# Kernel optimization log

Measured on AMD Instinct MI355X. Metric: run time of the kernel, lower is better.

Reference implementation:

```python
import jax, jax.numpy as jnp
import numpy as np

K, A, DIM = 1024, 16384, 512


def setup_inputs() -> dict:
    key = jax.random.key(0)
    ks = jax.random.split(key, 8)
    B, H, W = 2048, 8, 8
    z_t = jax.random.randint(ks[0], (B, H, W), 0, K, dtype=jnp.int64)
    z_tp1 = jax.random.randint(ks[1], (B, H, W), 0, K, dtype=jnp.int64)
    embed_w = jax.random.normal(ks[2], (K, DIM), dtype=jnp.float32) * 0.02
    # MLP: Linear(2*dim -> dim), GELU, Linear(dim -> dim)
    lim1 = 1.0 / np.sqrt(2 * DIM)
    w1 = jax.random.uniform(ks[3], (2 * DIM, DIM), minval=-lim1, maxval=lim1, dtype=jnp.float32)
    b1 = jax.random.uniform(ks[4], (DIM,), minval=-lim1, maxval=lim1, dtype=jnp.float32)
    lim2 = 1.0 / np.sqrt(DIM)
    w2 = jax.random.uniform(ks[5], (DIM, DIM), minval=-lim2, maxval=lim2, dtype=jnp.float32)
    b2 = jax.random.uniform(ks[6], (DIM,), minval=-lim2, maxval=lim2, dtype=jnp.float32)
    codebook_w = jax.random.normal(ks[7], (A, DIM), dtype=jnp.float32) * 0.02
    return {"z_t": z_t, "z_tp1": z_tp1, "embed_w": embed_w, "w1": w1, "b1": b1,
            "w2": w2, "b2": b2, "codebook_w": codebook_w}


def reference(z_t, z_tp1, embed_w, w1, b1, w2, b2, codebook_w):
    B = z_t.shape[0]
    # embed int code grids and mean-pool over H*W tokens -> [B, dim]
    e_t = embed_w[z_t.reshape(B, -1)].mean(axis=1)
    e_tp1 = embed_w[z_tp1.reshape(B, -1)].mean(axis=1)
    h = jnp.concatenate([e_t, e_tp1], axis=-1)          # [B, 2*dim]
    h = jax.nn.gelu(h @ w1 + b1, approximate=False)
    e = h @ w2 + b2                                      # [B, dim]
    # VQ: squared L2 distance to each code, argmin, gather
    d2 = (jnp.sum(e * e, axis=1, keepdims=True)
          - 2.0 * e @ codebook_w.T
          + jnp.sum(codebook_w * codebook_w, axis=1)[None, :])  # [B, A]
    ids = jnp.argmin(d2, axis=1)                         # [B]
    q = codebook_w[ids]                                  # [B, dim]
    return ids, q
```

## Files before the change

### kernel.cpp

```cpp
#include <hip/hip_runtime.h>
#include <hip/hip_bf16.h>

#define TOK 64
#define DIMC 512

typedef __attribute__((ext_vector_type(8))) short v8s;
typedef __attribute__((ext_vector_type(4))) float v4f;

__device__ __forceinline__ unsigned int f2ord(float f) {
  unsigned int u = __float_as_uint(f);
  return (u & 0x80000000u) ? ~u : (u | 0x80000000u);
}

__device__ __forceinline__ float gelu_exact(float x) {
  return 0.5f * x * (1.0f + erff(x * 0.70710678118654752440f));
}

__device__ __forceinline__ unsigned short f2bf(float x) {
  unsigned int u = __float_as_uint(x);
  return (unsigned short)((u + 0x7FFFu + ((u >> 16) & 1u)) >> 16);
}
__device__ __forceinline__ float bf2f(unsigned short h) {
  return __uint_as_float((unsigned int)h << 16);
}

__device__ __forceinline__ void gl2lds16(const void* g, void* l) {
  __builtin_amdgcn_global_load_lds((const __attribute__((address_space(1))) void*)g,
                                   (__attribute__((address_space(3))) void*)l,
                                   16, 0, 0);
}

__global__ __launch_bounds__(256) void k_prep(
    const int* __restrict__ zt, const int* __restrict__ ztp,
    const float* __restrict__ emb,
    unsigned short* __restrict__ hh, unsigned short* __restrict__ hl,
    unsigned long long* __restrict__ rowmin,
    const float* __restrict__ w1, unsigned short* __restrict__ w1th,
    unsigned short* __restrict__ w1tl,
    const float* __restrict__ w2, unsigned short* __restrict__ w2th,
    unsigned short* __restrict__ w2tl,
    const float* __restrict__ cb, unsigned short* __restrict__ ch,
    unsigned short* __restrict__ cl, float* __restrict__ cnorm) {
  __shared__ int codes[128];
  __shared__ float tbuf[32][33];
  const int bid = blockIdx.x;
  const int tid = threadIdx.x;

  if (bid < 2048) {
    const int b = bid;
    if (tid < 64) codes[tid] = zt[b * TOK + tid];
    else if (tid < 128) codes[tid] = ztp[b * TOK + (tid - 64)];
    if (tid == 0) rowmin[b] = 0xFFFFFFFFFFFFFFFFull;
    __syncthreads();
    const int half = tid >> 7;
    const int c4 = tid & 127;
    const float4* emb4 = (const float4*)emb;
    float4 s = make_float4(0.f, 0.f, 0.f, 0.f);
    #pragma unroll 8
    for (int t = 0; t < TOK; t++) {
      const int code = codes[half * TOK + t];
      const float4 v = emb4[code * 128 + c4];
      s.x += v.x; s.y += v.y; s.z += v.z; s.w += v.w;
    }
    const float inv = 1.0f / 64.0f;
    float f[4] = {s.x * inv, s.y * inv, s.z * inv, s.w * inv};
    unsigned short hi[4], lo[4];
    #pragma unroll
    for (int i = 0; i < 4; i++) {
      hi[i] = f2bf(f[i]);
      lo[i] = f2bf(f[i] - bf2f(hi[i]));
    }
    const int off = b * 1024 + half * 512 + c4 * 4;
    *(ushort4*)&hh[off] = make_ushort4(hi[0], hi[1], hi[2], hi[3]);
    *(ushort4*)&hl[off] = make_ushort4(lo[0], lo[1], lo[2], lo[3]);
  } else if (bid < 2816) {
    const float* w; unsigned short *wth, *wtl; int Kd, N, k0, n0;
    if (bid < 2560) {
      const int i = bid - 2048;
      w = w1; wth = w1th; wtl = w1tl; Kd = 1024; N = 512;
      k0 = (i & 31) * 32; n0 = (i >> 5) * 32;
    } else {
      const int i = bid - 2560;
      w = w2; wth = w2th; wtl = w2tl; Kd = 512; N = 512;
      k0 = (i & 15) * 32; n0 = (i >> 4) * 32;
    }
    const int c = tid & 31, r = tid >> 5;
    #pragma unroll
    for (int i = 0; i < 4; i++)
      tbuf[r + i * 8][c] = w[(size_t)(k0 + r + i * 8) * N + n0 + c];
    __syncthreads();
    #pragma unroll
    for (int i = 0; i < 4; i++) {
      const float v = tbuf[c][r + i * 8];
      const unsigned short hi = f2bf(v);
      const unsigned short lo = f2bf(v - bf2f(hi));
      wth[(size_t)(n0 + r + i * 8) * Kd + k0 + c] = hi;
      wtl[(size_t)(n0 + r + i * 8) * Kd + k0 + c] = lo;
    }
  } else {
    const int row = (bid - 2816) * 4 + (tid >> 6);
    const int lane = tid & 63;
    const float4* cb4 = (const float4*)cb;
    const float4 va = cb4[row * 128 + lane * 2];
    const float4 vb = cb4[row * 128 + lane * 2 + 1];
    float s = va.x * va.x + va.y * va.y + va.z * va.z + va.w * va.w
            + vb.x * vb.x + vb.y * vb.y + vb.z * vb.z + vb.w * vb.w;
    float f[8] = {va.x, va.y, va.z, va.w, vb.x, vb.y, vb.z, vb.w};
    unsigned short hi[8], lo[8];
    #pragma unroll
    for (int i = 0; i < 8; i++) {
      hi[i] = f2bf(f[i]);
      lo[i] = f2bf(f[i] - bf2f(hi[i]));
    }
    ushort4* chp = (ushort4*)&ch[row * DIMC + lane * 8];
    ushort4* clp = (ushort4*)&cl[row * DIMC + lane * 8];
    chp[0] = make_ushort4(hi[0], hi[1], hi[2], hi[3]);
    chp[1] = make_ushort4(hi[4], hi[5], hi[6], hi[7]);
    clp[0] = make_ushort4(lo[0], lo[1], lo[2], lo[3]);
    clp[1] = make_ushort4(lo[4], lo[5], lo[6], lo[7]);
    #pragma unroll
    for (int off = 32; off > 0; off >>= 1) s += __shfl_down(s, off);
    if (lane == 0) cnorm[row] = s;
  }
}

template <bool GELU>
__global__ __launch_bounds__(256) void k_gemm(const unsigned short* __restrict__ Ah_,
                                              const unsigned short* __restrict__ Al_,
                                              const unsigned short* __restrict__ Bh_,
                                              const unsigned short* __restrict__ Bl_,
                                              const float* __restrict__ bias,
                                              unsigned short* __restrict__ oh,
                                              unsigned short* __restrict__ ol,
                                              int Kd, int N) {
  __shared__ unsigned short AhS[2][32 * 32];
  __shared__ unsigned short AlS[2][32 * 32];
  __shared__ unsigned short BhS[2][64 * 32];
  __shared__ unsigned short BlS[2][64 * 32];

  const int tid = threadIdx.x;
  const int lane = tid & 63;
  const int wid = tid >> 6;
  const int m0 = blockIdx.x * 32;
  const int n0 = blockIdx.y * 64;

  const unsigned short* Ab_h = Ah_ + (size_t)m0 * Kd;
  const unsigned short* Ab_l = Al_ + (size_t)m0 * Kd;
  const unsigned short* Bb_h = Bh_ + (size_t)n0 * Kd;
  const unsigned short* Bb_l = Bl_ + (size_t)n0 * Kd;

  const int srow = lane >> 2;
  const int sk = (lane & 3) * 8;
  const int wm = wid >> 1, wn = wid & 1;
  const int fr = lane & 15;
  const int fq = (lane >> 4) * 8;

  v4f acc[2];
  acc[0] = (v4f)(0.f);
  acc[1] = (v4f)(0.f);

  auto stage = [&](int b, int k0) {
    #pragma unroll
    for (int u = 0; u < 3; u++) {
      const int i = wid * 3 + u;
      const unsigned short* gs; unsigned short* ls; int rbase;
      if (i < 2)      { gs = Ab_h; ls = AhS[b]; rbase = i * 16; }
      else if (i < 4) { gs = Ab_l; ls = AlS[b]; rbase = (i - 2) * 16; }
      else if (i < 8) { gs = Bb_h; ls = BhS[b]; rbase = (i - 4) * 16; }
      else            { gs = Bb_l; ls = BlS[b]; rbase = (i - 8) * 16; }
      gl2lds16(gs + (size_t)(rbase + srow) * Kd + k0 + sk, ls + rbase * 32);
    }
  };

  stage(0, 0);
  int cur = 0;
  for (int k0 = 0; k0 < Kd; k0 += 32) {
    __syncthreads();
    if (k0 + 32 < Kd) stage(cur ^ 1, k0 + 32);

    const int ar = (wm * 16 + fr) * 32 + fq;
    const v8s ah = *(const v8s*)&AhS[cur][ar];
    const v8s al = *(const v8s*)&AlS[cur][ar];
    #pragma unroll
    for (int nt = 0; nt < 2; nt++) {
      const int br = (wn * 32 + nt * 16 + fr) * 32 + fq;
      const v8s bh = *(const v8s*)&BhS[cur][br];
      const v8s bl = *(const v8s*)&BlS[cur][br];
      acc[nt] = __builtin_amdgcn_mfma_f32_16x16x32_bf16(ah, bh, acc[nt], 0, 0, 0);
      acc[nt] = __builtin_amdgcn_mfma_f32_16x16x32_bf16(ah, bl, acc[nt], 0, 0, 0);
      acc[nt] = __builtin_amdgcn_mfma_f32_16x16x32_bf16(al, bh, acc[nt], 0, 0, 0);
    }
    cur ^= 1;
  }

  const int col16 = lane & 15;
  const int q = lane >> 4;
  #pragma unroll
  for (int nt = 0; nt < 2; nt++) {
    const int col = n0 + wn * 32 + nt * 16 + col16;
    const float bv = bias[col];
    #pragma unroll
    for (int reg = 0; reg < 4; reg++) {
      const int row = m0 + wm * 16 + q * 4 + reg;
      float v = acc[nt][reg] + bv;
      if (GELU) v = gelu_exact(v);
      const unsigned short hi = f2bf(v);
      oh[(size_t)row * N + col] = hi;
      ol[(size_t)row * N + col] = f2bf(v - bf2f(hi));
    }
  }
}

__global__ __launch_bounds__(512, 2) void k_vq(const unsigned short* __restrict__ eh,
                                               const unsigned short* __restrict__ el,
                                               const unsigned short* __restrict__ ch,
                                               const unsigned short* __restrict__ cl,
                                               const float* __restrict__ cnorm,
                                               unsigned long long* __restrict__ rowmin) {
  __shared__ unsigned short lds[2 * 32768];

  const int tid = threadIdx.x;
  const int lane = tid & 63;
  const int wid = tid >> 6;
  const int bid = blockIdx.x;
  const int x = (bid >> 3) & 7;
  const int y = (((bid >> 6) & 7) << 3) | (bid & 7);
  const int r0 = x * 256;
  const int c0 = y * 256;

  const unsigned short* ehB = eh + (size_t)r0 * DIMC;
  const unsigned short* elB = el + (size_t)r0 * DIMC;
  const unsigned short* chB = ch + (size_t)c0 * DIMC;
  const unsigned short* clB = cl + (size_t)c0 * DIMC;

  const int srow = lane >> 2;
  const int sk = (lane & 3) * 8;
  const int wm = wid >> 1;
  const int wn = wid & 1;
  const int fr = lane & 15;
  const int q = lane >> 4;
  const int fq = q * 8;

  v4f acc[4][8];
  #pragma unroll
  for (int i = 0; i < 4; i++)
    #pragma unroll
    for (int jj = 0; jj < 8; jj++) acc[i][jj] = (v4f)(0.f);

  const unsigned short* gp[8];
  int lo_[8];
  #pragma unroll
  for (int u = 0; u < 8; u++) {
    const int i = wid * 8 + u;
    const unsigned short* gs; int off, rbase;
    if (i < 16)      { gs = ehB; off = 0;     rbase = i * 16; }
    else if (i < 32) { gs = elB; off = 8192;  rbase = (i - 16) * 16; }
    else if (i < 48) { gs = chB; off = 16384; rbase = (i - 32) * 16; }
    else             { gs = clB; off = 24576; rbase = (i - 48) * 16; }
    gp[u] = gs + (size_t)(rbase + srow) * DIMC + sk;
    lo_[u] = off + rbase * 32;
  }

  auto stage = [&](int buf, int k0) {
    #pragma unroll
    for (int u = 0; u < 8; u++)
      gl2lds16(gp[u] + k0, lds + buf * 32768 + lo_[u]);
  };

  stage(0, 0);
  __syncthreads();

  for (int t = 0; t < 16; ++t) {
    if (t < 15) stage((t + 1) & 1, (t + 1) * 32);

    const unsigned short* base = lds + (t & 1) * 32768;
    v8s ah[4], al[4];
    #pragma unroll
    for (int mt = 0; mt < 4; mt++) {
      const int ar = (wm * 64 + mt * 16 + fr) * 32 + fq;
      ah[mt] = *(const v8s*)&base[ar];
      al[mt] = *(const v8s*)&base[8192 + ar];
    }
    __builtin_amdgcn_s_setprio(1);
    #pragma unroll
    for (int nt = 0; nt < 8; nt++) {
      const int br = (wn * 128 + nt * 16 + fr) * 32 + fq;
      const v8s bh = *(const v8s*)&base[16384 + br];
      const v8s bl = *(const v8s*)&base[24576 + br];
      #pragma unroll
      for (int mt = 0; mt < 4; mt++) {
        acc[mt][nt] = __builtin_amdgcn_mfma_f32_16x16x32_bf16(ah[mt], bh, acc[mt][nt], 0, 0, 0);
        acc[mt][nt] = __builtin_amdgcn_mfma_f32_16x16x32_bf16(ah[mt], bl, acc[mt][nt], 0, 0, 0);
        acc[mt][nt] = __builtin_amdgcn_mfma_f32_16x16x32_bf16(al[mt], bh, acc[mt][nt], 0, 0, 0);
      }
    }
    __builtin_amdgcn_s_setprio(0);
    if (t < 15) __syncthreads();
  }

  const int col16 = lane & 15;
  float cn[8];
  #pragma unroll
  for (int nt = 0; nt < 8; nt++) cn[nt] = cnorm[c0 + wn * 128 + nt * 16 + col16];

  #pragma unroll
  for (int mt = 0; mt < 4; mt++) {
    #pragma unroll
    for (int reg = 0; reg < 4; reg++) {
      const int row = r0 + wm * 64 + mt * 16 + q * 4 + reg;
      float best = fmaf(-2.f, acc[mt][0][reg], cn[0]);
      int bid2 = c0 + wn * 128 + col16;
      #pragma unroll
      for (int nt = 1; nt < 8; nt++) {
        const float s = fmaf(-2.f, acc[mt][nt][reg], cn[nt]);
        const int id = c0 + wn * 128 + nt * 16 + col16;
        if (s < best) { best = s; bid2 = id; }
      }
      unsigned long long v =
          ((unsigned long long)f2ord(best) << 32) | (unsigned int)bid2;
      #pragma unroll
      for (int off = 8; off > 0; off >>= 1) {
        const unsigned long long o = __shfl_down(v, off, 16);
        if (o < v) v = o;
      }
      if (col16 == 0) atomicMin(&rowmin[row], v);
    }
  }
}

__global__ __launch_bounds__(64) void k_final(const unsigned long long* __restrict__ rowmin,
                                              const float* __restrict__ cb,
                                              float* __restrict__ out,
                                              int B) {
  const int b = blockIdx.x;
  const int t = threadIdx.x;
  const unsigned long long m = rowmin[b];
  const int id = (int)(unsigned int)(m & 0xFFFFFFFFull);
  if (t == 0) out[b] = (float)id;
  float4* q4 = (float4*)(out + B) + b * 128;
  const float4* cb4 = (const float4*)cb + (size_t)id * 128;
  q4[t] = cb4[t];
  q4[t + 64] = cb4[t + 64];
}

extern "C" void kernel_launch(void* const* d_in, const int* in_sizes, int n_in,
                              void* d_out, int out_size, void* d_ws, size_t ws_size,
                              hipStream_t stream) {
  const int* zt = (const int*)d_in[0];
  const int* ztp = (const int*)d_in[1];
  const float* emb = (const float*)d_in[2];
  const float* w1 = (const float*)d_in[3];
  const float* b1 = (const float*)d_in[4];
  const float* w2 = (const float*)d_in[5];
  const float* b2 = (const float*)d_in[6];
  const float* cb = (const float*)d_in[7];
  float* out = (float*)d_out;

  const int B = in_sizes[0] / TOK;
  const int A = in_sizes[7] / DIMC;

  char* p = (char*)d_ws;
  unsigned short* hh = (unsigned short*)p;  p += (size_t)B * 1024 * 2;
  unsigned short* hl = (unsigned short*)p;  p += (size_t)B * 1024 * 2;
  unsigned short* w1th = (unsigned short*)p; p += (size_t)512 * 1024 * 2;
  unsigned short* w1tl = (unsigned short*)p; p += (size_t)512 * 1024 * 2;
  unsigned short* w2th = (unsigned short*)p; p += (size_t)512 * 512 * 2;
  unsigned short* w2tl = (unsigned short*)p; p += (size_t)512 * 512 * 2;
  unsigned short* h1h = (unsigned short*)p; p += (size_t)B * DIMC * 2;
  unsigned short* h1l = (unsigned short*)p; p += (size_t)B * DIMC * 2;
  unsigned short* eh = (unsigned short*)p;  p += (size_t)B * DIMC * 2;
  unsigned short* el = (unsigned short*)p;  p += (size_t)B * DIMC * 2;
  unsigned short* ch = (unsigned short*)p;  p += (size_t)A * DIMC * 2;
  unsigned short* cl = (unsigned short*)p;  p += (size_t)A * DIMC * 2;
  float* cnorm = (float*)p;                 p += (size_t)A * 4;
  unsigned long long* rowmin = (unsigned long long*)p;

  k_prep<<<2816 + A / 4, 256, 0, stream>>>(zt, ztp, emb, hh, hl, rowmin,
                                           w1, w1th, w1tl, w2, w2th, w2tl,
                                           cb, ch, cl, cnorm);
  k_gemm<true><<<dim3(B / 32, 512 / 64), 256, 0, stream>>>(hh, hl, w1th, w1tl, b1, h1h, h1l, 1024, 512);
  k_gemm<false><<<dim3(B / 32, 512 / 64), 256, 0, stream>>>(h1h, h1l, w2th, w2tl, b2, eh, el, 512, 512);
  k_vq<<<(B / 256) * (A / 256), 512, 0, stream>>>(eh, el, ch, cl, cnorm, rowmin);
  k_final<<<B, 64, 0, stream>>>(rowmin, cb, out, B);
}
```

Measured before the change: 224.2 us.

## Split VQ distance MFMA loop into barrier-synchronized phases interleaving prefetch

Restructures the VQ distance GEMM main loop into four phases per k-step. Each phase loads two B tiles from LDS and spreads the next-tile global-to-LDS prefetch across the first two phases. Explicit s_barrier, waitcnt and sched_barrier calls replace __syncthreads so that waves stay in lockstep and memory issue interleaves with MFMA bursts, in the style of ping-pong scheduling. This adds many extra barriers per iteration, which could stall waves.

```diff
diff --git a/kernel.cpp b/kernel.cpp
--- a/kernel.cpp
+++ b/kernel.cpp
@@ -6,6 +6,8 @@
 
 typedef __attribute__((ext_vector_type(8))) short v8s;
 typedef __attribute__((ext_vector_type(4))) float v4f;
+
+#define MFMA16 __builtin_amdgcn_mfma_f32_16x16x32_bf16
 
 __device__ __forceinline__ unsigned int f2ord(float f) {
   unsigned int u = __float_as_uint(f);
@@ -186,9 +188,9 @@
       const int br = (wn * 32 + nt * 16 + fr) * 32 + fq;
       const v8s bh = *(const v8s*)&BhS[cur][br];
       const v8s bl = *(const v8s*)&BlS[cur][br];
-      acc[nt] = __builtin_amdgcn_mfma_f32_16x16x32_bf16(ah, bh, acc[nt], 0, 0, 0);
-      acc[nt] = __builtin_amdgcn_mfma_f32_16x16x32_bf16(ah, bl, acc[nt], 0, 0, 0);
-      acc[nt] = __builtin_amdgcn_mfma_f32_16x16x32_bf16(al, bh, acc[nt], 0, 0, 0);
+      acc[nt] = MFMA16(ah, bh, acc[nt], 0, 0, 0);
+      acc[nt] = MFMA16(ah, bl, acc[nt], 0, 0, 0);
+      acc[nt] = MFMA16(al, bh, acc[nt], 0, 0, 0);
     }
     cur ^= 1;
   }
@@ -261,19 +263,49 @@
     lo_[u] = off + rbase * 32;
   }
 
-  auto stage = [&](int buf, int k0) {
-    #pragma unroll
-    for (int u = 0; u < 8; u++)
-      gl2lds16(gp[u] + k0, lds + buf * 32768 + lo_[u]);
-  };
-
-  stage(0, 0);
-  __syncthreads();
-
+  #pragma unroll
+  for (int u = 0; u < 8; u++) gl2lds16(gp[u], lds + lo_[u]);
+  asm volatile("s_waitcnt vmcnt(0)" ::: "memory");
+  __builtin_amdgcn_s_barrier();
+
+#define VQ_PHASE(P, H)                                                        \
+  {                                                                           \
+    const int n0p = (wn * 128 + (2 * (P)) * 16 + fr) * 32 + fq;               \
+    const int n1p = (wn * 128 + (2 * (P) + 1) * 16 + fr) * 32 + fq;           \
+    const v8s bh0 = *(const v8s*)&base[16384 + n0p];                          \
+    const v8s bl0 = *(const v8s*)&base[24576 + n0p];                          \
+    const v8s bh1 = *(const v8s*)&base[16384 + n1p];                          \
+    const v8s bl1 = *(const v8s*)&base[24576 + n1p];                          \
+    if ((H) >= 0 && t < 15) {                                                 \
+      _Pragma("unroll")                                                       \
+      for (int u = (H) * 4; u < (H) * 4 + 4; u++)                             \
+        gl2lds16(gp[u] + kn, dbase + lo_[u]);                                 \
+    }                                                                         \
+    __builtin_amdgcn_s_barrier();                                             \
+    asm volatile("s_waitcnt lgkmcnt(0)" ::: "memory");                        \
+    __builtin_amdgcn_sched_barrier(0);                                        \
+    __builtin_amdgcn_s_setprio(1);                                            \
+    _Pragma("unroll")                                                         \
+    for (int mt = 0; mt < 4; mt++) {                                          \
+      acc[mt][2 * (P)] = MFMA16(ah[mt], bh0, acc[mt][2 * (P)], 0, 0, 0);      \
+      acc[mt][2 * (P)] = MFMA16(ah[mt], bl0, acc[mt][2 * (P)], 0, 0, 0);      \
+      acc[mt][2 * (P)] = MFMA16(al[mt], bh0, acc[mt][2 * (P)], 0, 0, 0);      \
+    }                                                                         \
+    _Pragma("unroll")                                                         \
+    for (int mt = 0; mt < 4; mt++) {                                          \
+      acc[mt][2 * (P) + 1] = MFMA16(ah[mt], bh1, acc[mt][2 * (P) + 1], 0, 0, 0); \
+      acc[mt][2 * (P) + 1] = MFMA16(ah[mt], bl1, acc[mt][2 * (P) + 1], 0, 0, 0); \
+      acc[mt][2 * (P) + 1] = MFMA16(al[mt], bh1, acc[mt][2 * (P) + 1], 0, 0, 0); \
+    }                                                                         \
+    __builtin_amdgcn_s_setprio(0);                                            \
+  }
+
+  #pragma unroll 2
   for (int t = 0; t < 16; ++t) {
-    if (t < 15) stage((t + 1) & 1, (t + 1) * 32);
-
     const unsigned short* base = lds + (t & 1) * 32768;
+    unsigned short* dbase = lds + ((t + 1) & 1) * 32768;
+    const int kn = (t + 1) * 32;
+
     v8s ah[4], al[4];
     #pragma unroll
     for (int mt = 0; mt < 4; mt++) {
@@ -281,22 +313,19 @@
       ah[mt] = *(const v8s*)&base[ar];
       al[mt] = *(const v8s*)&base[8192 + ar];
     }
-    __builtin_amdgcn_s_setprio(1);
-    #pragma unroll
-    for (int nt = 0; nt < 8; nt++) {
-      const int br = (wn * 128 + nt * 16 + fr) * 32 + fq;
-      const v8s bh = *(const v8s*)&base[16384 + br];
-      const v8s bl = *(const v8s*)&base[24576 + br];
-      #pragma unroll
-      for (int mt = 0; mt < 4; mt++) {
-        acc[mt][nt] = __builtin_amdgcn_mfma_f32_16x16x32_bf16(ah[mt], bh, acc[mt][nt], 0, 0, 0);
-        acc[mt][nt] = __builtin_amdgcn_mfma_f32_16x16x32_bf16(ah[mt], bl, acc[mt][nt], 0, 0, 0);
-        acc[mt][nt] = __builtin_amdgcn_mfma_f32_16x16x32_bf16(al[mt], bh, acc[mt][nt], 0, 0, 0);
-      }
-    }
-    __builtin_amdgcn_s_setprio(0);
-    if (t < 15) __syncthreads();
-  }
+    VQ_PHASE(0, 0)
+    __builtin_amdgcn_s_barrier();
+    VQ_PHASE(1, 1)
+    __builtin_amdgcn_s_barrier();
+    VQ_PHASE(2, -1)
+    __builtin_amdgcn_s_barrier();
+    VQ_PHASE(3, -1)
+    if (t < 15) {
+      asm volatile("s_waitcnt vmcnt(0)" ::: "memory");
+      __builtin_amdgcn_s_barrier();
+    }
+  }
+#undef VQ_PHASE
 
   const int col16 = lane & 15;
   float cn[8];
```

Measured after the change: 229.9 us. 2.5% more time.
